# Performance work log

Hardware: AMD Instinct MI355X
Metric: run time of the kernel (lower is better)

Reference implementation:

```python
import jax, jax.numpy as jnp
import numpy as np

RADIUS = 8
NUM_CORNERS = 500


def _dwconv(x, k2d, mode):
    # depthwise 2D conv on NCHW with explicit border padding (kornia-style)
    ph, pw = k2d.shape[0] // 2, k2d.shape[1] // 2
    xp = jnp.pad(x, ((0, 0), (0, 0), (ph, ph), (pw, pw)), mode=mode)
    C = x.shape[1]
    kern = jnp.broadcast_to(k2d[None, None], (C, 1, k2d.shape[0], k2d.shape[1])).astype(x.dtype)
    return jax.lax.conv_general_dilated(xp, kern, (1, 1), 'VALID',
                                        feature_group_count=C,
                                        dimension_numbers=('NCHW', 'OIHW', 'NCHW'))


def _gauss2d(k, sigma):
    x = jnp.arange(k, dtype=jnp.float32) - (k - 1) / 2.0
    g = jnp.exp(-(x * x) / (2.0 * sigma * sigma))
    g = g / g.sum()
    return jnp.outer(g, g)


def _nms2d(x):
    # kornia.feature.nms2d with (5,5) window: keep values equal to local max
    m = jax.lax.reduce_window(x, -jnp.inf, jax.lax.max, (1, 1, 5, 5), (1, 1, 1, 1), 'SAME')
    return x * (x == m).astype(x.dtype)


def _gftt(gray):
    # kornia CornerGFTT: sobel gradients (normalized /8, replicate pad),
    # structure tensor blurred with gaussian(7, sigma=1), min eigenvalue
    kx = jnp.array([[-1., 0., 1.], [-2., 0., 2.], [-1., 0., 1.]], jnp.float32) / 8.0
    dx = _dwconv(gray, kx, 'edge')
    dy = _dwconv(gray, kx.T, 'edge')
    g7 = _gauss2d(7, 1.0)
    dx2 = _dwconv(dx * dx, g7, 'reflect')
    dy2 = _dwconv(dy * dy, g7, 'reflect')
    dxy = _dwconv(dx * dy, g7, 'reflect')
    det = dx2 * dy2 - dxy * dxy
    tr = dx2 + dy2
    return 0.5 * (tr - jnp.sqrt(jnp.abs(tr * tr - 4.0 * det)))


def _laplacian5(x):
    # kornia laplacian kernel size 5, normalized by abs-sum (=48), reflect pad
    k = jnp.ones((5, 5), jnp.float32).at[2, 2].set(1.0 - 25.0)
    k = k / jnp.abs(k).sum()
    return _dwconv(x, k, 'reflect')


def _get_corners(imgs):
    B, _, H, W = imgs.shape
    r, N = RADIUS, NUM_CORNERS
    gray = 0.299 * imgs[:, :1] + 0.587 * imgs[:, 1:2] + 0.114 * imgs[:, 2:3]
    corners = _nms2d(_gftt(gray))
    # MaxPool2d(r, return_indices) + MaxUnpool2d(r): keep only per-block max
    blocks = corners.reshape(B, 1, H // r, r, W // r, r)
    bmax = blocks.max(axis=(3, 5), keepdims=True)
    unpooled = jnp.where(blocks == bmax, blocks, 0.0).reshape(B, 1, H, W)
    values, idx = jax.lax.top_k(unpooled.reshape(B, -1), N)   # [B,N]
    h, w = idx // W, idx % W
    b = jnp.repeat(jnp.arange(B), N)
    target = jnp.zeros((B, 1, H, W), imgs.dtype).at[b, 0, h.ravel(), w.ravel()].set(values.ravel())
    target = _nms2d(target)
    return (target > 0).astype(target.dtype)


def setup_inputs() -> dict:
    key = jax.random.key(0)
    k1, k2 = jax.random.split(key)
    scores_dense = jax.random.uniform(k1, (16, 1, 512, 512), dtype=jnp.float32)
    imgs = jax.random.uniform(k2, (16, 3, 512, 512), dtype=jnp.float32)
    return {"scores_dense": scores_dense, "imgs": imgs}


def reference(scores_dense, imgs):
    corners = _dwconv(_get_corners(imgs), _gauss2d(7, 1.0), 'reflect')
    lap = _laplacian5(scores_dense)
    logp = jnp.clip(jnp.log(scores_dense), -100.0)      # torch BCELoss clamps log at -100
    log1mp = jnp.clip(jnp.log1p(-scores_dense), -100.0)
    bce = -(corners * logp + (1.0 - corners) * log1mp).mean()
    return bce + (scores_dense * jnp.exp(-lap)).mean() * 10.0
```

## Files before the change

### kernel.cpp

```cpp
#include <hip/hip_runtime.h>
#include <math.h>

#define BB 16
#define HH 512
#define WW 512
#define HWP (HH*WW)
#define NPIX (BB*HWP)
#define HWP4 (HWP/4)
#define NG (NPIX/4)
#define NCORN 500
#define NSLOT 4096
#define OCAP 1024
#define NKEY (NSLOT+OCAP)
#define NKPT (NKEY/256)
#define NBL 4096

__device__ __constant__ float G7c[7] = {
    0.0044330482f, 0.0540055826f, 0.2420362294f, 0.3990502793f,
    0.2420362294f, 0.0540055826f, 0.0044330482f};

__device__ __forceinline__ int reflect_idx(int i, int n) {
    if (i < 0) i = -i;
    if (i >= n) i = 2 * n - 2 - i;
    return i;
}

__device__ __forceinline__ float w1d(int p, int o, int n) {
    float w = 0.f;
    int d = p - o;
    if (d >= -3 && d <= 3) w += G7c[d + 3];
    if (p >= 1 && p + o <= 3) w += G7c[3 - p - o];
    if (p <= n - 2 && p + o >= 2 * n - 5) w += G7c[2 * n + 1 - p - o];
    return w;
}

__global__ void k_gray(const float* __restrict__ imgs, float* __restrict__ gray) {
    int g = blockIdx.x * blockDim.x + threadIdx.x;
    if (g >= NG) return;
    int b = g / HWP4, r = g % HWP4;
    const float4* base = (const float4*)(imgs + (size_t)b * 3 * HWP);
    float4 R = base[r], G = base[r + HWP4], Bc = base[r + 2 * HWP4];
    float4 o;
    o.x = 0.299f * R.x + 0.587f * G.x + 0.114f * Bc.x;
    o.y = 0.299f * R.y + 0.587f * G.y + 0.114f * Bc.y;
    o.z = 0.299f * R.z + 0.587f * G.z + 0.114f * Bc.z;
    o.w = 0.299f * R.w + 0.587f * G.w + 0.114f * Bc.w;
    ((float4*)gray)[g] = o;
}

__global__ __launch_bounds__(256) void k_front(const float* __restrict__ gray,
                                               float* __restrict__ S) {
    int gid = blockIdx.x * 256 + threadIdx.x;
    int cstrip = gid & 127;
    int band = (gid >> 7) & 63;
    int b = gid >> 13;
    int x0 = cstrip * 4;
    int y0 = band * 8;
    const float* gb = gray + (size_t)b * HWP;
    float* Sb = S + (size_t)b * HWP;
    bool edgeL = (x0 == 0), edgeR = (x0 == 508);

    float aA[7][4], aC[7][4], aD[7][4];
#pragma unroll
    for (int s = 0; s < 7; ++s)
#pragma unroll
        for (int k = 0; k < 4; ++k) { aA[s][k] = 0.f; aC[s][k] = 0.f; aD[s][k] = 0.f; }

#pragma unroll
    for (int i = 0; i < 14; ++i) {
        int tp = y0 - 3 + i;
        int src = reflect_idx(tp, HH);
        int r0 = max(src - 1, 0), r2 = min(src + 1, HH - 1);
        float G[3][12];
        {
            const float* rw0 = gb + (size_t)r0 * WW;
            const float* rw1 = gb + (size_t)src * WW;
            const float* rw2 = gb + (size_t)r2 * WW;
            const float* rws[3] = {rw0, rw1, rw2};
#pragma unroll
            for (int r = 0; r < 3; ++r) {
                const float* rw = rws[r];
                float4 own = *(const float4*)(rw + x0);
                G[r][4] = own.x; G[r][5] = own.y; G[r][6] = own.z; G[r][7] = own.w;
                if (!edgeL) {
                    float4 lf = *(const float4*)(rw + x0 - 4);
                    G[r][0] = lf.x; G[r][1] = lf.y; G[r][2] = lf.z; G[r][3] = lf.w;
                } else {
                    G[r][0] = 0.f; G[r][1] = 0.f; G[r][2] = 0.f;
                    G[r][3] = own.x;
                }
                if (!edgeR) {
                    float4 rt = *(const float4*)(rw + x0 + 4);
                    G[r][8] = rt.x; G[r][9] = rt.y; G[r][10] = rt.z; G[r][11] = rt.w;
                } else {
                    G[r][8] = own.w;
                    G[r][9] = 0.f; G[r][10] = 0.f; G[r][11] = 0.f;
                }
            }
        }
        float pa[10], pc[10], pd[10];
#pragma unroll
        for (int j = 0; j < 10; ++j) {
            int gi = j + 1;
            float dx = (G[0][gi+1] - G[0][gi-1] + 2.f * (G[1][gi+1] - G[1][gi-1])
                        + G[2][gi+1] - G[2][gi-1]) * 0.125f;
            float dy = (G[2][gi-1] - G[0][gi-1] + 2.f * (G[2][gi] - G[0][gi])
                        + G[2][gi+1] - G[0][gi+1]) * 0.125f;
            pa[j] = dx * dx; pc[j] = dy * dy; pd[j] = dx * dy;
        }
        if (edgeL) {
            pa[2] = pa[4]; pc[2] = pc[4]; pd[2] = pd[4];
            pa[1] = pa[5]; pc[1] = pc[5]; pd[1] = pd[5];
            pa[0] = pa[6]; pc[0] = pc[6]; pd[0] = pd[6];
        }
        if (edgeR) {
            pa[7] = pa[5]; pc[7] = pc[5]; pd[7] = pd[5];
            pa[8] = pa[4]; pc[8] = pc[4]; pd[8] = pd[4];
            pa[9] = pa[3]; pc[9] = pc[3]; pd[9] = pd[3];
        }
        float hA[4], hC[4], hD[4];
#pragma unroll
        for (int k = 0; k < 4; ++k) {
            float A = 0.f, C = 0.f, D = 0.f;
#pragma unroll
            for (int t = 0; t < 7; ++t) {
                float w = G7c[t];
                A += w * pa[k + t]; C += w * pc[k + t]; D += w * pd[k + t];
            }
            hA[k] = A; hC[k] = C; hD[k] = D;
        }
#pragma unroll
        for (int d2 = 0; d2 < 7; ++d2) {
            int l = i - 6 + d2;
            if (l < 0 || l > 7) continue;
            float w = G7c[6 - d2];
#pragma unroll
            for (int k = 0; k < 4; ++k) {
                aA[l % 7][k] += w * hA[k];
                aC[l % 7][k] += w * hC[k];
                aD[l % 7][k] += w * hD[k];
            }
        }
        if (i >= 6) {
            int l = i - 6, s = l % 7;
            float4 o; float* po = (float*)&o;
#pragma unroll
            for (int k = 0; k < 4; ++k) {
                float det = aA[s][k] * aC[s][k] - aD[s][k] * aD[s][k];
                float tr = aA[s][k] + aC[s][k];
                po[k] = 0.5f * (tr - sqrtf(fabsf(tr * tr - 4.f * det)));
                aA[s][k] = 0.f; aC[s][k] = 0.f; aD[s][k] = 0.f;
            }
            *(float4*)(Sb + (size_t)(y0 + l) * WW + x0) = o;
        }
    }
}

__global__ void k_cand2(const float* __restrict__ S, float* __restrict__ sval,
                        int* __restrict__ sidx, int* __restrict__ ocnt) {
    __shared__ float tile[4][12][12];
    int wave = threadIdx.x >> 6, lane = threadIdx.x & 63;
    int tx = blockIdx.x * 4 + wave;
    int ty = blockIdx.y;
    int b = blockIdx.z;
    const float* sb = S + (size_t)b * HWP;
    for (int t = lane; t < 144; t += 64) {
        int r = t / 12, c = t % 12;
        int yy = min(max(ty * 8 - 2 + r, 0), HH - 1);
        int xx = min(max(tx * 8 - 2 + c, 0), WW - 1);
        tile[wave][r][c] = sb[yy * WW + xx];
    }
    __syncthreads();
    int ly = lane >> 3, lx = lane & 7;
    float v = tile[wave][ly + 2][lx + 2];
    float m = -INFINITY;
#pragma unroll
    for (int dy = 0; dy < 5; ++dy)
#pragma unroll
        for (int dx = 0; dx < 5; ++dx)
            m = fmaxf(m, tile[wave][ly + dy][lx + dx]);
    float cval = (v == m) ? v : 0.f;
    int y = ty * 8 + ly, x = tx * 8 + lx;
    float tm = cval;
#pragma unroll
    for (int off = 32; off; off >>= 1)
        tm = fmaxf(tm, __shfl_xor(tm, off));
    unsigned long long mask = __ballot(cval == tm && cval > 0.f);
    int slot = ty * 64 + tx;
    if (mask) {
        int first = __ffsll(mask) - 1;
        if (lane == first) {
            sval[b * NKEY + slot] = cval;
            sidx[b * NKEY + slot] = y * WW + x;
        } else if ((mask >> lane) & 1ull) {
            int pos = atomicAdd(&ocnt[b], 1);
            if (pos < OCAP) {
                sval[b * NKEY + NSLOT + pos] = cval;
                sidx[b * NKEY + NSLOT + pos] = y * WW + x;
            }
        }
    } else if (lane == 0) {
        sval[b * NKEY + slot] = 0.f;
        sidx[b * NKEY + slot] = 0;
    }
}

__global__ __launch_bounds__(256) void k_sel(const float* __restrict__ sval,
                       const int* __restrict__ sidx, const int* __restrict__ ocnt,
                       unsigned long long* __restrict__ selK) {
    __shared__ int shw[4];
    __shared__ int shtot;
    int b = blockIdx.x;
    int n = NSLOT + min(ocnt[b], OCAP);
    unsigned long long keys[NKPT];
    int cnt = 0;
#pragma unroll
    for (int t = 0; t < NKPT; ++t) {
        int i = threadIdx.x + t * 256;
        unsigned long long k = 0ull;
        if (i < n) {
            float v = sval[b * NKEY + i];
            if (v > 0.f) {
                unsigned int ix = (unsigned int)sidx[b * NKEY + i];
                k = ((unsigned long long)__float_as_uint(v) << 32) |
                    (unsigned long long)(~ix);
                cnt++;
            }
        }
        keys[t] = k;
    }
    int wid = threadIdx.x >> 6;
    {
        int c = cnt;
#pragma unroll
        for (int off = 32; off; off >>= 1) c += __shfl_down(c, off);
        if ((threadIdx.x & 63) == 0) shw[wid] = c;
        __syncthreads();
        if (threadIdx.x == 0) shtot = shw[0] + shw[1] + shw[2] + shw[3];
        __syncthreads();
    }
    int target = min(NCORN, shtot);
    unsigned long long T = 0ull;
    for (int bit = 63; bit >= 0; --bit) {
        unsigned long long cand = T | (1ull << bit);
        int c = 0;
#pragma unroll
        for (int t = 0; t < NKPT; ++t) c += (keys[t] >= cand) ? 1 : 0;
#pragma unroll
        for (int off = 32; off; off >>= 1) c += __shfl_down(c, off);
        __syncthreads();
        if ((threadIdx.x & 63) == 0) shw[wid] = c;
        __syncthreads();
        int tot = shw[0] + shw[1] + shw[2] + shw[3];
        if (tot >= target) T = cand;
    }
    if (threadIdx.x == 0) selK[b] = T;
}

__global__ void k_post(const float* __restrict__ sval, const int* __restrict__ sidx,
                       const int* __restrict__ ocnt, const unsigned long long* __restrict__ selK,
                       float* __restrict__ corners) {
    int gid = blockIdx.x * blockDim.x + threadIdx.x;
    if (gid >= BB * NKEY) return;
    int b = gid / NKEY, s = gid % NKEY;
    int novf = min(ocnt[b], OCAP);
    if (s >= NSLOT + novf) return;
    float v = sval[gid];
    if (v <= 0.f) return;
    unsigned int ix = (unsigned int)sidx[gid];
    unsigned long long K = selK[b];
    unsigned long long k = ((unsigned long long)__float_as_uint(v) << 32) |
                           (unsigned long long)(~ix);
    if (k < K) return;
    int y = (int)(ix >> 9), x = (int)(ix & 511);
    const float* bsv = sval + b * NKEY;
    const int* bsi = sidx + b * NKEY;
    bool sup = false;
    int ty0 = max(y - 2, 0) >> 3, ty1 = min(y + 2, HH - 1) >> 3;
    int tx0 = max(x - 2, 0) >> 3, tx1 = min(x + 2, WW - 1) >> 3;
    for (int ty = ty0; ty <= ty1 && !sup; ++ty)
        for (int tx = tx0; tx <= tx1 && !sup; ++tx) {
            int s2 = ty * 64 + tx;
            float v2 = bsv[s2];
            if (v2 <= v) continue;
            int ix2 = bsi[s2];
            unsigned long long k2 = ((unsigned long long)__float_as_uint(v2) << 32) |
                                    (unsigned long long)(~(unsigned int)ix2);
            if (k2 < K) continue;
            int y2 = ix2 >> 9, x2 = ix2 & 511;
            if (abs(y2 - y) <= 2 && abs(x2 - x) <= 2) sup = true;
        }
    for (int j = 0; j < novf && !sup; ++j) {
        float v2 = bsv[NSLOT + j];
        if (v2 <= v) continue;
        int ix2 = bsi[NSLOT + j];
        unsigned long long k2 = ((unsigned long long)__float_as_uint(v2) << 32) |
                                (unsigned long long)(~(unsigned int)ix2);
        if (k2 < K) continue;
        int y2 = ix2 >> 9, x2 = ix2 & 511;
        if (abs(y2 - y) <= 2 && abs(x2 - x) <= 2) sup = true;
    }
    if (sup) return;
    float* cb = corners + (size_t)b * HWP;
    if (y >= 3 && y <= HH - 4 && x >= 3 && x <= WW - 4) {
#pragma unroll
        for (int j = -3; j <= 3; ++j) {
            float wy = G7c[j + 3];
#pragma unroll
            for (int i = -3; i <= 3; ++i)
                atomicAdd(cb + (y + j) * WW + (x + i), wy * G7c[i + 3]);
        }
    } else {
        int oy0 = max(y - 6, 0), oy1 = min(y + 6, HH - 1);
        int ox0 = max(x - 6, 0), ox1 = min(x + 6, WW - 1);
        for (int oy = oy0; oy <= oy1; ++oy) {
            float wy = w1d(y, oy, HH);
            if (wy == 0.f) continue;
            for (int ox = ox0; ox <= ox1; ++ox) {
                float wx = w1d(x, ox, WW);
                if (wx != 0.f) atomicAdd(cb + oy * WW + ox, wy * wx);
            }
        }
    }
}

__global__ void k_loss(const float* __restrict__ scores, const float* __restrict__ corners,
                       float* __restrict__ partial) {
    int g = blockIdx.x * blockDim.x + threadIdx.x;
    float bce = 0.f, reg = 0.f;
    if (g < NG) {
        int b = g / HWP4, rem = g % HWP4;
        int p = rem * 4, y = p >> 9, x0 = p & 511;
        const float* sb = scores + (size_t)b * HWP;
        float s25[4] = {0.f, 0.f, 0.f, 0.f};
        float pv[4];
        if (x0 >= 4 && x0 <= 504) {
#pragma unroll
            for (int j = -2; j <= 2; ++j) {
                int yy = reflect_idx(y + j, HH);
                const float4* q = (const float4*)(sb + (size_t)yy * WW + x0 - 4);
                float4 qa = q[0], qb = q[1], qc = q[2];
                float f[12] = {qa.x,qa.y,qa.z,qa.w, qb.x,qb.y,qb.z,qb.w, qc.x,qc.y,qc.z,qc.w};
#pragma unroll
                for (int k = 0; k < 4; ++k)
                    s25[k] += f[k+2] + f[k+3] + f[k+4] + f[k+5] + f[k+6];
                if (j == 0) { pv[0]=f[4]; pv[1]=f[5]; pv[2]=f[6]; pv[3]=f[7]; }
            }
        } else {
            for (int k = 0; k < 4; ++k) {
                int x = x0 + k;
                float s = 0.f;
                for (int j = -2; j <= 2; ++j) {
                    const float* r = sb + (size_t)reflect_idx(y + j, HH) * WW;
                    for (int i = -2; i <= 2; ++i)
                        s += r[reflect_idx(x + i, WW)];
                }
                s25[k] = s;
                pv[k] = sb[(size_t)y * WW + x];
            }
        }
        float4 c4 = ((const float4*)corners)[g];
        float cv[4] = {c4.x, c4.y, c4.z, c4.w};
#pragma unroll
        for (int k = 0; k < 4; ++k) {
            float pp = pv[k], cc = cv[k];
            float lp = __logf(pp);
            lp = (lp > -100.f) ? lp : -100.f;
            float l1p = __logf(1.f - pp);
            l1p = (l1p > -100.f) ? l1p : -100.f;
            bce += -(cc * lp + (1.f - cc) * l1p);
            float lap = (s25[k] - 25.f * pp) * (1.0f / 48.0f);
            reg += pp * __expf(-lap);
        }
    }
#pragma unroll
    for (int off = 32; off; off >>= 1) {
        bce += __shfl_down(bce, off);
        reg += __shfl_down(reg, off);
    }
    __shared__ float wb[4], wr[4];
    int wid = threadIdx.x >> 6, lid = threadIdx.x & 63;
    if (lid == 0) { wb[wid] = bce; wr[wid] = reg; }
    __syncthreads();
    if (threadIdx.x == 0) {
        float tb = 0.f, tr = 0.f;
        for (int w = 0; w < 4; ++w) { tb += wb[w]; tr += wr[w]; }
        partial[blockIdx.x] = tb;
        partial[NBL + blockIdx.x] = tr;
    }
}

__global__ void k_reduce(const float* __restrict__ partial, float* __restrict__ out) {
    float tb = 0.f, tr = 0.f;
    for (int i = threadIdx.x; i < NBL; i += blockDim.x) {
        tb += partial[i];
        tr += partial[NBL + i];
    }
#pragma unroll
    for (int off = 32; off; off >>= 1) {
        tb += __shfl_down(tb, off);
        tr += __shfl_down(tr, off);
    }
    __shared__ float wb[4], wr[4];
    int wid = threadIdx.x >> 6, lid = threadIdx.x & 63;
    if (lid == 0) { wb[wid] = tb; wr[wid] = tr; }
    __syncthreads();
    if (threadIdx.x == 0) {
        float sb = 0.f, sr = 0.f;
        for (int w = 0; w < 4; ++w) { sb += wb[w]; sr += wr[w]; }
        float invN = 1.0f / (float)NPIX;
        out[0] = sb * invN + sr * invN * 10.0f;
    }
}

extern "C" void kernel_launch(void* const* d_in, const int* in_sizes, int n_in,
                              void* d_out, int out_size, void* d_ws, size_t ws_size,
                              hipStream_t stream) {
    const float* scores = (const float*)d_in[0];
    const float* imgs   = (const float*)d_in[1];
    float* out = (float*)d_out;

    float* ws = (float*)d_ws;
    float* A0 = ws;
    float* A1 = ws + (size_t)NPIX;
    float* A2 = ws + 2 * (size_t)NPIX;
    float* sval = ws + 3 * (size_t)NPIX;
    int*   sidx = (int*)(sval + (size_t)BB * NKEY);
    int*   ocnt = (int*)(sidx + (size_t)BB * NKEY);
    unsigned long long* selK = (unsigned long long*)(ocnt + BB);
    float* partial = (float*)(selK + BB);

    const int T = 256;
    const int GG = NG / T;

    k_gray <<<GG, T, 0, stream>>>(imgs, A0);
    k_front<<<BB * 64 * 128 / T, T, 0, stream>>>(A0, A1);

    hipMemsetAsync(ocnt, 0, BB * sizeof(int), stream);
    dim3 gcand(16, 64, BB);
    k_cand2<<<gcand, 256, 0, stream>>>(A1, sval, sidx, ocnt);

    hipMemsetAsync(A2, 0, (size_t)NPIX * sizeof(float), stream);

    k_sel<<<BB, 256, 0, stream>>>(sval, sidx, ocnt, selK);
    const int GS = (BB * NKEY + T - 1) / T;
    k_post<<<GS, T, 0, stream>>>(sval, sidx, ocnt, selK, A2);

    k_loss  <<<NBL, T, 0, stream>>>(scores, A2, partial);
    k_reduce<<<1, 256, 0, stream>>>(partial, out);
}
```

Baseline: 293.6 us.

## Scatter corner BCE contributions directly and tile front/loss stencils in shared memory

The dense corner map buffer and its memset and atomic scatter are removed. BCE is split algebraically into a dense -log(1-p) term plus a sparse per-corner sum of w*(log p - log(1-p)) computed inside k_post. k_front moves from per-thread register strips to shared-memory staged separable passes over 64x16 tiles. k_loss stages rows in LDS to compute the 5x5 box sum separably. This drops a full-image memset, write and read along with tens of thousands of atomics, at the cost of extra LDS traffic and barriers.

New measurement: 266.6 us. 1.1x faster.

```diff
diff --git a/kernel.cpp b/kernel.cpp
--- a/kernel.cpp
+++ b/kernel.cpp
@@ -13,7 +13,8 @@
 #define OCAP 1024
 #define NKEY (NSLOT+OCAP)
 #define NKPT (NKEY/256)
-#define NBL 4096
+#define NBL 2048
+#define NPOSTB 320
 
 __device__ __constant__ float G7c[7] = {
     0.0044330482f, 0.0540055826f, 0.2420362294f, 0.3990502793f,
@@ -50,109 +51,70 @@
 
 __global__ __launch_bounds__(256) void k_front(const float* __restrict__ gray,
                                                float* __restrict__ S) {
-    int gid = blockIdx.x * 256 + threadIdx.x;
-    int cstrip = gid & 127;
-    int band = (gid >> 7) & 63;
-    int b = gid >> 13;
-    int x0 = cstrip * 4;
-    int y0 = band * 8;
+    __shared__ float gt[24][72];
+    __shared__ float pA[22][70], pC[22][70], pD[22][70];
+    __shared__ float hA[22][64], hC[22][64], hD[22][64];
+    int x0 = blockIdx.x * 64;
+    int y0 = blockIdx.y * 16;
+    int b = blockIdx.z;
     const float* gb = gray + (size_t)b * HWP;
-    float* Sb = S + (size_t)b * HWP;
-    bool edgeL = (x0 == 0), edgeR = (x0 == 508);
-
-    float aA[7][4], aC[7][4], aD[7][4];
-#pragma unroll
-    for (int s = 0; s < 7; ++s)
-#pragma unroll
-        for (int k = 0; k < 4; ++k) { aA[s][k] = 0.f; aC[s][k] = 0.f; aD[s][k] = 0.f; }
-
-#pragma unroll
-    for (int i = 0; i < 14; ++i) {
-        int tp = y0 - 3 + i;
-        int src = reflect_idx(tp, HH);
-        int r0 = max(src - 1, 0), r2 = min(src + 1, HH - 1);
-        float G[3][12];
-        {
-            const float* rw0 = gb + (size_t)r0 * WW;
-            const float* rw1 = gb + (size_t)src * WW;
-            const float* rw2 = gb + (size_t)r2 * WW;
-            const float* rws[3] = {rw0, rw1, rw2};
-#pragma unroll
-            for (int r = 0; r < 3; ++r) {
-                const float* rw = rws[r];
-                float4 own = *(const float4*)(rw + x0);
-                G[r][4] = own.x; G[r][5] = own.y; G[r][6] = own.z; G[r][7] = own.w;
-                if (!edgeL) {
-                    float4 lf = *(const float4*)(rw + x0 - 4);
-                    G[r][0] = lf.x; G[r][1] = lf.y; G[r][2] = lf.z; G[r][3] = lf.w;
-                } else {
-                    G[r][0] = 0.f; G[r][1] = 0.f; G[r][2] = 0.f;
-                    G[r][3] = own.x;
-                }
-                if (!edgeR) {
-                    float4 rt = *(const float4*)(rw + x0 + 4);
-                    G[r][8] = rt.x; G[r][9] = rt.y; G[r][10] = rt.z; G[r][11] = rt.w;
-                } else {
-                    G[r][8] = own.w;
-                    G[r][9] = 0.f; G[r][10] = 0.f; G[r][11] = 0.f;
-                }
+    int tid = threadIdx.x;
+
+    for (int idx = tid; idx < 24 * 72; idx += 256) {
+        int r = idx / 72, c = idx % 72;
+        int gy = min(max(y0 - 4 + r, 0), HH - 1);
+        int gx = min(max(x0 - 4 + c, 0), WW - 1);
+        gt[r][c] = gb[gy * WW + gx];
+    }
+    __syncthreads();
+
+    for (int idx = tid; idx < 22 * 70; idx += 256) {
+        int r = idx / 70, c = idx % 70;
+        int py = y0 - 3 + r, px = x0 - 3 + c;
+        if (py >= 0 && py < HH && px >= 0 && px < WW) {
+            float g00 = gt[r][c],   g01 = gt[r][c+1],   g02 = gt[r][c+2];
+            float g10 = gt[r+1][c],                     g12 = gt[r+1][c+2];
+            float g20 = gt[r+2][c], g21 = gt[r+2][c+1], g22 = gt[r+2][c+2];
+            float dx = (g02 - g00 + 2.f * (g12 - g10) + g22 - g20) * 0.125f;
+            float dy = (g20 - g00 + 2.f * (g21 - g01) + g22 - g02) * 0.125f;
+            pA[r][c] = dx * dx; pC[r][c] = dy * dy; pD[r][c] = dx * dy;
+        }
+    }
+    __syncthreads();
+
+    for (int idx = tid; idx < 22 * 64; idx += 256) {
+        int r = idx / 64, c = idx % 64;
+        int py = y0 - 3 + r;
+        if (py >= 0 && py < HH) {
+            int ox = x0 + c;
+            float A = 0.f, C = 0.f, D = 0.f;
+#pragma unroll
+            for (int t = 0; t < 7; ++t) {
+                int px = reflect_idx(ox - 3 + t, WW);
+                int lc = px - (x0 - 3);
+                float w = G7c[t];
+                A += w * pA[r][lc]; C += w * pC[r][lc]; D += w * pD[r][lc];
             }
-        }
-        float pa[10], pc[10], pd[10];
-#pragma unroll
-        for (int j = 0; j < 10; ++j) {
-            int gi = j + 1;
-            float dx = (G[0][gi+1] - G[0][gi-1] + 2.f * (G[1][gi+1] - G[1][gi-1])
-                        + G[2][gi+1] - G[2][gi-1]) * 0.125f;
-            float dy = (G[2][gi-1] - G[0][gi-1] + 2.f * (G[2][gi] - G[0][gi])
-                        + G[2][gi+1] - G[0][gi+1]) * 0.125f;
-            pa[j] = dx * dx; pc[j] = dy * dy; pd[j] = dx * dy;
-        }
-        if (edgeL) {
-            pa[2] = pa[4]; pc[2] = pc[4]; pd[2] = pd[4];
-            pa[1] = pa[5]; pc[1] = pc[5]; pd[1] = pd[5];
-            pa[0] = pa[6]; pc[0] = pc[6]; pd[0] = pd[6];
-        }
-        if (edgeR) {
-            pa[7] = pa[5]; pc[7] = pc[5]; pd[7] = pd[5];
-            pa[8] = pa[4]; pc[8] = pc[4]; pd[8] = pd[4];
-            pa[9] = pa[3]; pc[9] = pc[3]; pd[9] = pd[3];
-        }
-        float hA[4], hC[4], hD[4];
-#pragma unroll
-        for (int k = 0; k < 4; ++k) {
-            float A = 0.f, C = 0.f, D = 0.f;
-#pragma unroll
-            for (int t = 0; t < 7; ++t) {
-                float w = G7c[t];
-                A += w * pa[k + t]; C += w * pc[k + t]; D += w * pd[k + t];
-            }
-            hA[k] = A; hC[k] = C; hD[k] = D;
-        }
-#pragma unroll
-        for (int d2 = 0; d2 < 7; ++d2) {
-            int l = i - 6 + d2;
-            if (l < 0 || l > 7) continue;
-            float w = G7c[6 - d2];
-#pragma unroll
-            for (int k = 0; k < 4; ++k) {
-                aA[l % 7][k] += w * hA[k];
-                aC[l % 7][k] += w * hC[k];
-                aD[l % 7][k] += w * hD[k];
-            }
-        }
-        if (i >= 6) {
-            int l = i - 6, s = l % 7;
-            float4 o; float* po = (float*)&o;
-#pragma unroll
-            for (int k = 0; k < 4; ++k) {
-                float det = aA[s][k] * aC[s][k] - aD[s][k] * aD[s][k];
-                float tr = aA[s][k] + aC[s][k];
-                po[k] = 0.5f * (tr - sqrtf(fabsf(tr * tr - 4.f * det)));
-                aA[s][k] = 0.f; aC[s][k] = 0.f; aD[s][k] = 0.f;
-            }
-            *(float4*)(Sb + (size_t)(y0 + l) * WW + x0) = o;
-        }
+            hA[r][c] = A; hC[r][c] = C; hD[r][c] = D;
+        }
+    }
+    __syncthreads();
+
+    for (int idx = tid; idx < 16 * 64; idx += 256) {
+        int r = idx / 64, c = idx % 64;
+        int oy = y0 + r;
+        float A = 0.f, C = 0.f, D = 0.f;
+#pragma unroll
+        for (int t = 0; t < 7; ++t) {
+            int py = reflect_idx(oy - 3 + t, HH);
+            int lr = py - (y0 - 3);
+            float w = G7c[t];
+            A += w * hA[lr][c]; C += w * hC[lr][c]; D += w * hD[lr][c];
+        }
+        float det = A * C - D * D;
+        float tr = A + C;
+        S[(size_t)b * HWP + (size_t)oy * WW + x0 + c] =
+            0.5f * (tr - sqrtf(fabsf(tr * tr - 4.f * det)));
     }
 }
 
@@ -257,159 +219,166 @@
     if (threadIdx.x == 0) selK[b] = T;
 }
 
-__global__ void k_post(const float* __restrict__ sval, const int* __restrict__ sidx,
-                       const int* __restrict__ ocnt, const unsigned long long* __restrict__ selK,
-                       float* __restrict__ corners) {
-    int gid = blockIdx.x * blockDim.x + threadIdx.x;
-    if (gid >= BB * NKEY) return;
-    int b = gid / NKEY, s = gid % NKEY;
+__global__ __launch_bounds__(256) void k_post(const float* __restrict__ sval,
+                       const int* __restrict__ sidx, const int* __restrict__ ocnt,
+                       const unsigned long long* __restrict__ selK,
+                       const float* __restrict__ scores,
+                       float* __restrict__ partialC) {
+    int gid = blockIdx.x * 256 + threadIdx.x;
+    int b = gid / NKEY, s = gid - b * NKEY;
     int novf = min(ocnt[b], OCAP);
-    if (s >= NSLOT + novf) return;
-    float v = sval[gid];
-    if (v <= 0.f) return;
-    unsigned int ix = (unsigned int)sidx[gid];
-    unsigned long long K = selK[b];
-    unsigned long long k = ((unsigned long long)__float_as_uint(v) << 32) |
-                           (unsigned long long)(~ix);
-    if (k < K) return;
-    int y = (int)(ix >> 9), x = (int)(ix & 511);
-    const float* bsv = sval + b * NKEY;
-    const int* bsi = sidx + b * NKEY;
-    bool sup = false;
-    int ty0 = max(y - 2, 0) >> 3, ty1 = min(y + 2, HH - 1) >> 3;
-    int tx0 = max(x - 2, 0) >> 3, tx1 = min(x + 2, WW - 1) >> 3;
-    for (int ty = ty0; ty <= ty1 && !sup; ++ty)
-        for (int tx = tx0; tx <= tx1 && !sup; ++tx) {
-            int s2 = ty * 64 + tx;
-            float v2 = bsv[s2];
-            if (v2 <= v) continue;
-            int ix2 = bsi[s2];
-            unsigned long long k2 = ((unsigned long long)__float_as_uint(v2) << 32) |
-                                    (unsigned long long)(~(unsigned int)ix2);
-            if (k2 < K) continue;
-            int y2 = ix2 >> 9, x2 = ix2 & 511;
-            if (abs(y2 - y) <= 2 && abs(x2 - x) <= 2) sup = true;
-        }
-    for (int j = 0; j < novf && !sup; ++j) {
-        float v2 = bsv[NSLOT + j];
-        if (v2 <= v) continue;
-        int ix2 = bsi[NSLOT + j];
-        unsigned long long k2 = ((unsigned long long)__float_as_uint(v2) << 32) |
-                                (unsigned long long)(~(unsigned int)ix2);
-        if (k2 < K) continue;
-        int y2 = ix2 >> 9, x2 = ix2 & 511;
-        if (abs(y2 - y) <= 2 && abs(x2 - x) <= 2) sup = true;
-    }
-    if (sup) return;
-    float* cb = corners + (size_t)b * HWP;
-    if (y >= 3 && y <= HH - 4 && x >= 3 && x <= WW - 4) {
-#pragma unroll
-        for (int j = -3; j <= 3; ++j) {
-            float wy = G7c[j + 3];
-#pragma unroll
-            for (int i = -3; i <= 3; ++i)
-                atomicAdd(cb + (y + j) * WW + (x + i), wy * G7c[i + 3]);
-        }
-    } else {
-        int oy0 = max(y - 6, 0), oy1 = min(y + 6, HH - 1);
-        int ox0 = max(x - 6, 0), ox1 = min(x + 6, WW - 1);
-        for (int oy = oy0; oy <= oy1; ++oy) {
-            float wy = w1d(y, oy, HH);
-            if (wy == 0.f) continue;
-            for (int ox = ox0; ox <= ox1; ++ox) {
-                float wx = w1d(x, ox, WW);
-                if (wx != 0.f) atomicAdd(cb + oy * WW + ox, wy * wx);
+    float contrib = 0.f;
+    float v = (s < NSLOT + novf) ? sval[gid] : 0.f;
+    if (v > 0.f) {
+        unsigned int ix = (unsigned int)sidx[gid];
+        unsigned long long K = selK[b];
+        unsigned long long k = ((unsigned long long)__float_as_uint(v) << 32) |
+                               (unsigned long long)(~ix);
+        if (k >= K) {
+            int y = (int)(ix >> 9), x = (int)(ix & 511);
+            const float* bsv = sval + b * NKEY;
+            const int* bsi = sidx + b * NKEY;
+            bool sup = false;
+            int ty0 = max(y - 2, 0) >> 3, ty1 = min(y + 2, HH - 1) >> 3;
+            int tx0 = max(x - 2, 0) >> 3, tx1 = min(x + 2, WW - 1) >> 3;
+            for (int ty = ty0; ty <= ty1 && !sup; ++ty)
+                for (int tx = tx0; tx <= tx1 && !sup; ++tx) {
+                    int s2 = ty * 64 + tx;
+                    float v2 = bsv[s2];
+                    if (v2 <= v) continue;
+                    int ix2 = bsi[s2];
+                    unsigned long long k2 = ((unsigned long long)__float_as_uint(v2) << 32) |
+                                            (unsigned long long)(~(unsigned int)ix2);
+                    if (k2 < K) continue;
+                    int y2 = ix2 >> 9, x2 = ix2 & 511;
+                    if (abs(y2 - y) <= 2 && abs(x2 - x) <= 2) sup = true;
+                }
+            for (int j = 0; j < novf && !sup; ++j) {
+                float v2 = bsv[NSLOT + j];
+                if (v2 <= v) continue;
+                int ix2 = bsi[NSLOT + j];
+                unsigned long long k2 = ((unsigned long long)__float_as_uint(v2) << 32) |
+                                        (unsigned long long)(~(unsigned int)ix2);
+                if (k2 < K) continue;
+                int y2 = ix2 >> 9, x2 = ix2 & 511;
+                if (abs(y2 - y) <= 2 && abs(x2 - x) <= 2) sup = true;
             }
-        }
-    }
-}
-
-__global__ void k_loss(const float* __restrict__ scores, const float* __restrict__ corners,
-                       float* __restrict__ partial) {
-    int g = blockIdx.x * blockDim.x + threadIdx.x;
-    float bce = 0.f, reg = 0.f;
-    if (g < NG) {
-        int b = g / HWP4, rem = g % HWP4;
-        int p = rem * 4, y = p >> 9, x0 = p & 511;
-        const float* sb = scores + (size_t)b * HWP;
-        float s25[4] = {0.f, 0.f, 0.f, 0.f};
-        float pv[4];
-        if (x0 >= 4 && x0 <= 504) {
-#pragma unroll
-            for (int j = -2; j <= 2; ++j) {
-                int yy = reflect_idx(y + j, HH);
-                const float4* q = (const float4*)(sb + (size_t)yy * WW + x0 - 4);
-                float4 qa = q[0], qb = q[1], qc = q[2];
-                float f[12] = {qa.x,qa.y,qa.z,qa.w, qb.x,qb.y,qb.z,qb.w, qc.x,qc.y,qc.z,qc.w};
-#pragma unroll
-                for (int k = 0; k < 4; ++k)
-                    s25[k] += f[k+2] + f[k+3] + f[k+4] + f[k+5] + f[k+6];
-                if (j == 0) { pv[0]=f[4]; pv[1]=f[5]; pv[2]=f[6]; pv[3]=f[7]; }
+            if (!sup) {
+                const float* sb = scores + (size_t)b * HWP;
+                if (y >= 3 && y <= HH - 4 && x >= 3 && x <= WW - 4) {
+#pragma unroll
+                    for (int j = -3; j <= 3; ++j) {
+                        float wy = G7c[j + 3];
+#pragma unroll
+                        for (int i = -3; i <= 3; ++i) {
+                            float w = wy * G7c[i + 3];
+                            float p = sb[(y + j) * WW + (x + i)];
+                            float lp = fmaxf(__logf(p), -100.f);
+                            float l1p = fmaxf(__logf(1.f - p), -100.f);
+                            contrib += w * (lp - l1p);
+                        }
+                    }
+                } else {
+                    int oy0 = max(y - 6, 0), oy1 = min(y + 6, HH - 1);
+                    int ox0 = max(x - 6, 0), ox1 = min(x + 6, WW - 1);
+                    for (int oy = oy0; oy <= oy1; ++oy) {
+                        float wy = w1d(y, oy, HH);
+                        if (wy == 0.f) continue;
+                        for (int ox = ox0; ox <= ox1; ++ox) {
+                            float wx = w1d(x, ox, WW);
+                            if (wx == 0.f) continue;
+                            float p = sb[oy * WW + ox];
+                            float lp = fmaxf(__logf(p), -100.f);
+                            float l1p = fmaxf(__logf(1.f - p), -100.f);
+                            contrib += wy * wx * (lp - l1p);
+                        }
+                    }
+                }
             }
-        } else {
-            for (int k = 0; k < 4; ++k) {
-                int x = x0 + k;
-                float s = 0.f;
-                for (int j = -2; j <= 2; ++j) {
-                    const float* r = sb + (size_t)reflect_idx(y + j, HH) * WW;
-                    for (int i = -2; i <= 2; ++i)
-                        s += r[reflect_idx(x + i, WW)];
-                }
-                s25[k] = s;
-                pv[k] = sb[(size_t)y * WW + x];
-            }
-        }
-        float4 c4 = ((const float4*)corners)[g];
-        float cv[4] = {c4.x, c4.y, c4.z, c4.w};
-#pragma unroll
-        for (int k = 0; k < 4; ++k) {
-            float pp = pv[k], cc = cv[k];
-            float lp = __logf(pp);
-            lp = (lp > -100.f) ? lp : -100.f;
-            float l1p = __logf(1.f - pp);
-            l1p = (l1p > -100.f) ? l1p : -100.f;
-            bce += -(cc * lp + (1.f - cc) * l1p);
-            float lap = (s25[k] - 25.f * pp) * (1.0f / 48.0f);
-            reg += pp * __expf(-lap);
-        }
+        }
+    }
+#pragma unroll
+    for (int off = 32; off; off >>= 1) contrib += __shfl_down(contrib, off);
+    __shared__ float wsum[4];
+    int wid = threadIdx.x >> 6;
+    if ((threadIdx.x & 63) == 0) wsum[wid] = contrib;
+    __syncthreads();
+    if (threadIdx.x == 0)
+        partialC[blockIdx.x] = wsum[0] + wsum[1] + wsum[2] + wsum[3];
+}
+
+__global__ __launch_bounds__(256) void k_loss(const float* __restrict__ scores,
+                                              float* __restrict__ partial) {
+    __shared__ float st[8][520];
+    __shared__ float h5[8][512];
+    int b = blockIdx.x >> 7;
+    int rg = blockIdx.x & 127;
+    int y0 = rg * 4;
+    const float* sb = scores + (size_t)b * HWP;
+    int tid = threadIdx.x;
+    for (int idx = tid; idx < 8 * 516; idx += 256) {
+        int i = idx / 516, c = idx % 516;
+        int gy = reflect_idx(y0 - 2 + i, HH);
+        int gx = reflect_idx(c - 2, WW);
+        st[i][c] = sb[gy * WW + gx];
+    }
+    __syncthreads();
+    for (int idx = tid; idx < 8 * 512; idx += 256) {
+        int i = idx >> 9, x = idx & 511;
+        h5[i][x] = st[i][x] + st[i][x + 1] + st[i][x + 2] + st[i][x + 3] + st[i][x + 4];
+    }
+    __syncthreads();
+    float a_loc = 0.f, b_loc = 0.f;
+#pragma unroll
+    for (int k = 0; k < 8; ++k) {
+        int idx = tid + k * 256;
+        int r = idx >> 9, x = idx & 511;
+        float p = st[r + 2][x + 2];
+        float s25 = h5[r][x] + h5[r + 1][x] + h5[r + 2][x] + h5[r + 3][x] + h5[r + 4][x];
+        float l1p = fmaxf(__logf(1.f - p), -100.f);
+        a_loc -= l1p;
+        float lap = (s25 - 25.f * p) * (1.0f / 48.0f);
+        b_loc += p * __expf(-lap);
     }
 #pragma unroll
     for (int off = 32; off; off >>= 1) {
-        bce += __shfl_down(bce, off);
-        reg += __shfl_down(reg, off);
-    }
-    __shared__ float wb[4], wr[4];
+        a_loc += __shfl_down(a_loc, off);
+        b_loc += __shfl_down(b_loc, off);
+    }
+    __shared__ float wa[4], wbs[4];
+    int wid = threadIdx.x >> 6;
+    if ((threadIdx.x & 63) == 0) { wa[wid] = a_loc; wbs[wid] = b_loc; }
+    __syncthreads();
+    if (threadIdx.x == 0) {
+        partial[blockIdx.x] = wa[0] + wa[1] + wa[2] + wa[3];
+        partial[NBL + blockIdx.x] = wbs[0] + wbs[1] + wbs[2] + wbs[3];
+    }
+}
+
+__global__ void k_reduce(const float* __restrict__ partial, float* __restrict__ out) {
+    float ta = 0.f, tb = 0.f, tc = 0.f;
+    for (int i = threadIdx.x; i < NBL; i += blockDim.x) {
+        ta += partial[i];
+        tb += partial[NBL + i];
+    }
+    for (int i = threadIdx.x; i < NPOSTB; i += blockDim.x)
+        tc += partial[2 * NBL + i];
+#pragma unroll
+    for (int off = 32; off; off >>= 1) {
+        ta += __shfl_down(ta, off);
+        tb += __shfl_down(tb, off);
+        tc += __shfl_down(tc, off);
+    }
+    __shared__ float wa[4], wb[4], wc[4];
     int wid = threadIdx.x >> 6, lid = threadIdx.x & 63;
-    if (lid == 0) { wb[wid] = bce; wr[wid] = reg; }
+    if (lid == 0) { wa[wid] = ta; wb[wid] = tb; wc[wid] = tc; }
     __syncthreads();
     if (threadIdx.x == 0) {
-        float tb = 0.f, tr = 0.f;
-        for (int w = 0; w < 4; ++w) { tb += wb[w]; tr += wr[w]; }
-        partial[blockIdx.x] = tb;
-        partial[NBL + blockIdx.x] = tr;
-    }
-}
-
-__global__ void k_reduce(const float* __restrict__ partial, float* __restrict__ out) {
-    float tb = 0.f, tr = 0.f;
-    for (int i = threadIdx.x; i < NBL; i += blockDim.x) {
-        tb += partial[i];
-        tr += partial[NBL + i];
-    }
-#pragma unroll
-    for (int off = 32; off; off >>= 1) {
-        tb += __shfl_down(tb, off);
-        tr += __shfl_down(tr, off);
-    }
-    __shared__ float wb[4], wr[4];
-    int wid = threadIdx.x >> 6, lid = threadIdx.x & 63;
-    if (lid == 0) { wb[wid] = tb; wr[wid] = tr; }
-    __syncthreads();
-    if (threadIdx.x == 0) {
-        float sb = 0.f, sr = 0.f;
-        for (int w = 0; w < 4; ++w) { sb += wb[w]; sr += wr[w]; }
+        float A = wa[0] + wa[1] + wa[2] + wa[3];
+        float Bv = wb[0] + wb[1] + wb[2] + wb[3];
+        float C = wc[0] + wc[1] + wc[2] + wc[3];
         float invN = 1.0f / (float)NPIX;
-        out[0] = sb * invN + sr * invN * 10.0f;
+        out[0] = (A - C) * invN + 10.0f * Bv * invN;
     }
 }
 
@@ -423,8 +392,7 @@
     float* ws = (float*)d_ws;
     float* A0 = ws;
     float* A1 = ws + (size_t)NPIX;
-    float* A2 = ws + 2 * (size_t)NPIX;
-    float* sval = ws + 3 * (size_t)NPIX;
+    float* sval = ws + 2 * (size_t)NPIX;
     int*   sidx = (int*)(sval + (size_t)BB * NKEY);
     int*   ocnt = (int*)(sidx + (size_t)BB * NKEY);
     unsigned long long* selK = (unsigned long long*)(ocnt + BB);
@@ -434,18 +402,15 @@
     const int GG = NG / T;
 
     k_gray <<<GG, T, 0, stream>>>(imgs, A0);
-    k_front<<<BB * 64 * 128 / T, T, 0, stream>>>(A0, A1);
+    k_front<<<dim3(8, 32, BB), T, 0, stream>>>(A0, A1);
 
     hipMemsetAsync(ocnt, 0, BB * sizeof(int), stream);
     dim3 gcand(16, 64, BB);
     k_cand2<<<gcand, 256, 0, stream>>>(A1, sval, sidx, ocnt);
 
-    hipMemsetAsync(A2, 0, (size_t)NPIX * sizeof(float), stream);
-
     k_sel<<<BB, 256, 0, stream>>>(sval, sidx, ocnt, selK);
-    const int GS = (BB * NKEY + T - 1) / T;
-    k_post<<<GS, T, 0, stream>>>(sval, sidx, ocnt, selK, A2);
-
-    k_loss  <<<NBL, T, 0, stream>>>(scores, A2, partial);
+    k_post<<<NPOSTB, 256, 0, stream>>>(sval, sidx, ocnt, selK, scores,
+                                       partial + 2 * NBL);
+    k_loss<<<NBL, T, 0, stream>>>(scores, partial);
     k_reduce<<<1, 256, 0, stream>>>(partial, out);
 }
```
